# Kernel tuning notes

Measured on AMD Instinct MI355X. Metric: run time of the kernel, lower is better.

## Reference

```python
import jax, jax.numpy as jnp
import numpy as np

BS = 1024
D = 64            # hidden_dim
S = 16            # neighbor_samples
HOPS = 2          # context_hops
AGG = 1.0         # agg_param
N_ENT = 200000
N_EDGE = 2000000
N_REL = 16


def setup_inputs() -> dict:
    key = jax.random.key(0)
    ks = jax.random.split(key, 10)
    return {
        "relations":    jax.random.randint(ks[0], (BS,), 0, N_REL),
        "entity_pairs": jax.random.randint(ks[1], (BS, 2), 0, N_ENT),
        "train_edges":  jax.random.randint(ks[2], (BS,), 0, N_EDGE),
        "entity2edges": jax.random.randint(ks[3], (N_ENT, S), 0, N_EDGE),
        "edge2entities": jax.random.randint(ks[4], (N_EDGE, 2), 0, N_ENT),
        "edge2relation": jax.random.randint(ks[5], (N_EDGE,), 0, N_REL),
        "relation_emb": jax.random.normal(ks[6], (N_REL, D), jnp.float32) * (1.0 / D ** 0.5),
        "entity_emb":   jax.random.normal(ks[7], (N_ENT, D), jnp.float32) * (1.0 / D ** 0.5),
        "scorer_w":     jax.random.normal(ks[8], (D, 1), jnp.float32) * 0.1,
        "scorer_b":     jnp.zeros((1,), jnp.float32),
    }


def reference(relations, entity_pairs, train_edges, entity2edges, edge2entities,
              edge2relation, relation_emb, entity_emb, scorer_w, scorer_b):
    bs = relations.shape[0]
    dtype = relation_emb.dtype

    # ---- _get_entity_neighbors_and_masks (train mode) ----
    edges_list = [relations]          # hop-0 "edges" are the relation ids
    nodes_list = []
    mask_list = []
    te = train_edges[:, None]         # the edge to predict is masked out
    for i in range(HOPS):
        if i == 0:
            neighbor_entities = entity_pairs                      # [bs, 2]
        else:
            # entities at the two endpoints of every previous-hop edge
            neighbor_entities = edge2entities[edges_list[-1]].reshape(bs, -1, 2)
        nodes_list.append(neighbor_entities)
        neighbor_edges = entity2edges[neighbor_entities.reshape(bs, -1)].reshape(bs, -1)
        edges_list.append(neighbor_edges)
        mask_list.append((neighbor_edges != te).astype(dtype))    # (edge - train_edge) != 0

    # ---- embedding lookups ----
    entity_vectors = [entity_emb[n] for n in nodes_list]
    edge_vectors = [relation_emb[edges_list[0]]]                  # [bs, D]
    for edges in edges_list[1:]:
        edge_vectors.append(relation_emb[edge2relation[edges]])

    # ---- iterative MeanAggregator hops (self_included=True) ----
    for i in range(HOPS):
        next_edge_vectors = []
        for hop in range(HOPS - i):
            self_vec = edge_vectors[hop].reshape(bs, -1, D)              # [bs, m, D]
            nev = entity_vectors[hop].reshape(bs, -1, 2, D)              # [bs, m, 2, D]
            nbv = edge_vectors[hop + 1].reshape(bs, -1, 2, S, D)         # [bs, m, 2, S, D]
            m = mask_list[hop].reshape(bs, -1, 2, S, 1)                  # [bs, m, 2, S, 1]
            nei_nums = jnp.sum(m, axis=-2)                               # [bs, m, 2, 1]
            nei_nums = jnp.where(nei_nums == 0, jnp.ones_like(nei_nums), nei_nums)
            edge_agg = jnp.sum(nbv * m, axis=-2) / nei_nums              # masked mean over S
            neighbor_vectors = nev + AGG * edge_agg                      # [bs, m, 2, D]
            self_vec = self_vec + AGG * jnp.mean(neighbor_vectors, axis=-2)
            next_edge_vectors.append(self_vec)
        edge_vectors = next_edge_vectors

    out = edge_vectors[0].reshape(bs, D)
    scores = out @ scorer_w + scorer_b                                   # mlp scorer
    return scores[:, 0]
```

## Files before the change

kernel.cpp:

```cpp
#include <hip/hip_runtime.h>


#define DIM 64
#define NS 16
#define NREL 16

__global__ __launch_bounds__(512, 8) void transmatch_main(
    const int* __restrict__ relations,
    const int* __restrict__ entity_pairs,
    const int* __restrict__ train_edges,
    const int* __restrict__ entity2edges,
    const int* __restrict__ edge2entities,
    const int* __restrict__ edge2relation,
    const float* __restrict__ relation_emb,
    const float* __restrict__ entity_emb,
    const float* __restrict__ scorer_w,
    const float* __restrict__ scorer_b,
    float* __restrict__ out)
{
    __shared__ float RwL[NREL];
    __shared__ float wL[DIM];
    __shared__ int   node_l[64];
    __shared__ int   m0i[32];
    __shared__ float c0s[2];
    __shared__ float ews[2];
    __shared__ float rw0s[2];
    __shared__ float wavesum[8];

    const int b    = blockIdx.x;
    const int t    = threadIdx.x;
    const int lane = t & 63;
    const int wave = t >> 6;
    const int te   = train_edges[b];

    if (t < DIM) wL[t] = scorer_w[t];

    int rel1 = 0, m0 = 0;
    if (wave == 0 && lane < 32) {
        const int p    = lane >> 4;
        const int e    = entity_pairs[b * 2 + p];
        const int edge = entity2edges[e * NS + (lane & 15)];
        m0   = (edge != te) ? 1 : 0;
        rel1 = edge2relation[edge];
        const int2 nn = reinterpret_cast<const int2*>(edge2entities)[edge];
        reinterpret_cast<int2*>(node_l)[lane] = nn;
        m0i[lane] = m0;
        int c = m0;
        c += __shfl_xor(c, 1); c += __shfl_xor(c, 2);
        c += __shfl_xor(c, 4); c += __shfl_xor(c, 8);
        if ((lane & 15) == 0) c0s[p] = (float)c;
    } else if (wave == 1) {
        const int p  = lane >> 5;
        const int e  = entity_pairs[b * 2 + p];
        const int k  = lane & 31;
        const float2 ev = reinterpret_cast<const float2*>(entity_emb)[e * 32 + k];
        float v = ev.x * scorer_w[2 * k] + ev.y * scorer_w[2 * k + 1];
        v += __shfl_xor(v, 1); v += __shfl_xor(v, 2); v += __shfl_xor(v, 4);
        v += __shfl_xor(v, 8); v += __shfl_xor(v, 16);
        if (k == 0) ews[p] = v;
    } else if (wave == 2) {
        const int r = lane >> 2, seg = lane & 3;
        const float4* R4 = reinterpret_cast<const float4*>(relation_emb);
        const float4* W4 = reinterpret_cast<const float4*>(scorer_w);
        float v = 0.0f;
        #pragma unroll
        for (int k = 0; k < 4; ++k) {
            const float4 rr = R4[r * 16 + seg * 4 + k];
            const float4 ww = W4[seg * 4 + k];
            v = fmaf(rr.x, ww.x, v); v = fmaf(rr.y, ww.y, v);
            v = fmaf(rr.z, ww.z, v); v = fmaf(rr.w, ww.w, v);
        }
        v += __shfl_xor(v, 1); v += __shfl_xor(v, 2);
        if (seg == 0) RwL[r] = v;
    }
    __syncthreads();

    if (wave == 0 && lane < 32) {
        float rv = m0 ? RwL[rel1] : 0.0f;
        rv += __shfl_xor(rv, 1); rv += __shfl_xor(rv, 2);
        rv += __shfl_xor(rv, 4); rv += __shfl_xor(rv, 8);
        if ((lane & 15) == 0) rw0s[lane >> 4] = rv;
    }

    {
        const int n    = t >> 3;
        const int h    = t & 7;
        const int node = node_l[n];

        const int2 ed = reinterpret_cast<const int2*>(entity2edges)[node * 8 + h];
        const int ra = edge2relation[ed.x];
        const int rb = edge2relation[ed.y];

        const float4* E4  = reinterpret_cast<const float4*>(entity_emb);
        const float4* wL4 = reinterpret_cast<const float4*>(wL);
        const float4 ev0 = E4[node * 16 + h * 2];
        const float4 ev1 = E4[node * 16 + h * 2 + 1];
        const float4 w0  = wL4[h * 2];
        const float4 w1  = wL4[h * 2 + 1];
        float dotp = 0.0f;
        dotp = fmaf(ev0.x, w0.x, dotp); dotp = fmaf(ev0.y, w0.y, dotp);
        dotp = fmaf(ev0.z, w0.z, dotp); dotp = fmaf(ev0.w, w0.w, dotp);
        dotp = fmaf(ev1.x, w1.x, dotp); dotp = fmaf(ev1.y, w1.y, dotp);
        dotp = fmaf(ev1.z, w1.z, dotp); dotp = fmaf(ev1.w, w1.w, dotp);

        int cnt = 0; float rws = 0.0f;
        if (ed.x != te) { cnt++; rws += RwL[ra]; }
        if (ed.y != te) { cnt++; rws += RwL[rb]; }

        dotp += __shfl_xor(dotp, 1); dotp += __shfl_xor(dotp, 2); dotp += __shfl_xor(dotp, 4);
        rws  += __shfl_xor(rws, 1);  rws  += __shfl_xor(rws, 2);  rws  += __shfl_xor(rws, 4);
        cnt  += __shfl_xor(cnt, 1);  cnt  += __shfl_xor(cnt, 2);  cnt  += __shfl_xor(cnt, 4);

        float v = 0.0f;
        if (h == 0 && m0i[n >> 1])
            v = dotp + rws / (float)max(cnt, 1);

        v += __shfl_xor(v, 8); v += __shfl_xor(v, 16); v += __shfl_xor(v, 32);
        if (lane == 0) wavesum[wave] = v;
    }
    __syncthreads();

    if (t == 0) {
        const float i0 = 1.0f / fmaxf(c0s[0], 1.0f);
        const float i1 = 1.0f / fmaxf(c0s[1], 1.0f);
        const float S0 = wavesum[0] + wavesum[1] + wavesum[2] + wavesum[3];
        const float S1 = wavesum[4] + wavesum[5] + wavesum[6] + wavesum[7];
        const int   r0 = relations[b];
        out[b] = scorer_b[0] + RwL[r0]
               + ews[0] + i0 * rw0s[0] + 0.25f * i0 * S0
               + ews[1] + i1 * rw0s[1] + 0.25f * i1 * S1;
    }
}

extern "C" void kernel_launch(void* const* d_in, const int* in_sizes, int n_in,
                              void* d_out, int out_size, void* d_ws, size_t ws_size,
                              hipStream_t stream) {
    const int*   relations     = (const int*)d_in[0];
    const int*   entity_pairs  = (const int*)d_in[1];
    const int*   train_edges   = (const int*)d_in[2];
    const int*   entity2edges  = (const int*)d_in[3];
    const int*   edge2entities = (const int*)d_in[4];
    const int*   edge2relation = (const int*)d_in[5];
    const float* relation_emb  = (const float*)d_in[6];
    const float* entity_emb    = (const float*)d_in[7];
    const float* scorer_w      = (const float*)d_in[8];
    const float* scorer_b      = (const float*)d_in[9];
    float* out = (float*)d_out;

    const int bs = in_sizes[0];

    transmatch_main<<<bs, 512, 0, stream>>>(
        relations, entity_pairs, train_edges, entity2edges, edge2entities,
        edge2relation, relation_emb, entity_emb, scorer_w, scorer_b, out);
}
```

Before: 24.17 us.

## Pack edge2relation into 4-bit nibbles and use nontemporal gather loads

Adds a pre-pass kernel that compresses the 2M-entry edge2relation table into 4-bit packed words in workspace, so the main kernel's random relation lookups touch a much smaller table. The main kernel's gathers from edge2entities, entity2edges and entity_emb switch to nontemporal loads to reduce cache pollution. In exchange, every call now streams the full 8 MB edge2relation array through an extra kernel, which likely outweighs the savings on a kernel that only does about 1024 blocks of random gathers. The packing also assumes relation ids fit in 4 bits.

```diff
diff --git a/kernel.cpp b/kernel.cpp
--- a/kernel.cpp
+++ b/kernel.cpp
@@ -5,17 +5,48 @@
 #define NS 16
 #define NREL 16
 
-__global__ __launch_bounds__(512, 8) void transmatch_main(
+typedef float f32x4 __attribute__((ext_vector_type(4)));
+typedef int   i32x2 __attribute__((ext_vector_type(2)));
+
+__global__ __launch_bounds__(256) void pack_nib_kernel(
+    const int* __restrict__ e2r, unsigned int* __restrict__ nib, int n) {
+    const int tid = blockIdx.x * blockDim.x + threadIdx.x;
+    const int i = tid * 8;
+    if (i + 7 < n) {
+        const int4 a = *reinterpret_cast<const int4*>(e2r + i);
+        const int4 b = *reinterpret_cast<const int4*>(e2r + i + 4);
+        unsigned int w =  (unsigned int)(a.x & 15)
+                       | ((unsigned int)(a.y & 15) << 4)
+                       | ((unsigned int)(a.z & 15) << 8)
+                       | ((unsigned int)(a.w & 15) << 12)
+                       | ((unsigned int)(b.x & 15) << 16)
+                       | ((unsigned int)(b.y & 15) << 20)
+                       | ((unsigned int)(b.z & 15) << 24)
+                       | ((unsigned int)(b.w & 15) << 28);
+        nib[tid] = w;
+    } else if (i < n) {
+        unsigned int w = 0;
+        for (int k = 0; k < 8 && i + k < n; ++k)
+            w |= ((unsigned int)(e2r[i + k] & 15)) << (4 * k);
+        nib[tid] = w;
+    }
+}
+
+__device__ __forceinline__ int rel4(const unsigned int* __restrict__ nib, int e) {
+    return (int)((nib[e >> 3] >> ((e & 7) << 2)) & 15u);
+}
+
+__global__ __launch_bounds__(512) void transmatch_main(
     const int* __restrict__ relations,
     const int* __restrict__ entity_pairs,
     const int* __restrict__ train_edges,
     const int* __restrict__ entity2edges,
     const int* __restrict__ edge2entities,
-    const int* __restrict__ edge2relation,
     const float* __restrict__ relation_emb,
     const float* __restrict__ entity_emb,
     const float* __restrict__ scorer_w,
     const float* __restrict__ scorer_b,
+    const unsigned int* __restrict__ nib,
     float* __restrict__ out)
 {
     __shared__ float RwL[NREL];
@@ -41,9 +72,11 @@
         const int e    = entity_pairs[b * 2 + p];
         const int edge = entity2edges[e * NS + (lane & 15)];
         m0   = (edge != te) ? 1 : 0;
-        rel1 = edge2relation[edge];
-        const int2 nn = reinterpret_cast<const int2*>(edge2entities)[edge];
-        reinterpret_cast<int2*>(node_l)[lane] = nn;
+        rel1 = rel4(nib, edge);
+        const i32x2 nn = __builtin_nontemporal_load(
+            reinterpret_cast<const i32x2*>(edge2entities) + edge);
+        node_l[2 * lane]     = nn.x;
+        node_l[2 * lane + 1] = nn.y;
         m0i[lane] = m0;
         int c = m0;
         c += __shfl_xor(c, 1); c += __shfl_xor(c, 2);
@@ -87,16 +120,17 @@
         const int h    = t & 7;
         const int node = node_l[n];
 
-        const int2 ed = reinterpret_cast<const int2*>(entity2edges)[node * 8 + h];
-        const int ra = edge2relation[ed.x];
-        const int rb = edge2relation[ed.y];
+        const i32x2 ed = __builtin_nontemporal_load(
+            reinterpret_cast<const i32x2*>(entity2edges) + (node * 8 + h));
+        const int ra = rel4(nib, ed.x);
+        const int rb = rel4(nib, ed.y);
 
-        const float4* E4  = reinterpret_cast<const float4*>(entity_emb);
+        const f32x4* E4 = reinterpret_cast<const f32x4*>(entity_emb);
         const float4* wL4 = reinterpret_cast<const float4*>(wL);
-        const float4 ev0 = E4[node * 16 + h * 2];
-        const float4 ev1 = E4[node * 16 + h * 2 + 1];
-        const float4 w0  = wL4[h * 2];
-        const float4 w1  = wL4[h * 2 + 1];
+        const f32x4 ev0 = __builtin_nontemporal_load(E4 + (node * 16 + h * 2));
+        const f32x4 ev1 = __builtin_nontemporal_load(E4 + (node * 16 + h * 2 + 1));
+        const float4 w0 = wL4[h * 2];
+        const float4 w1 = wL4[h * 2 + 1];
         float dotp = 0.0f;
         dotp = fmaf(ev0.x, w0.x, dotp); dotp = fmaf(ev0.y, w0.y, dotp);
         dotp = fmaf(ev0.z, w0.z, dotp); dotp = fmaf(ev0.w, w0.w, dotp);
@@ -147,9 +181,16 @@
     const float* scorer_b      = (const float*)d_in[9];
     float* out = (float*)d_out;
 
-    const int bs = in_sizes[0];
+    const int bs     = in_sizes[0];
+    const int n_edge = in_sizes[5];
+    const int n_words = (n_edge + 7) / 8;
+
+    unsigned int* nib = (unsigned int*)d_ws;
+    const int pack_threads = n_words;
+    pack_nib_kernel<<<(pack_threads + 255) / 256, 256, 0, stream>>>(
+        edge2relation, nib, n_edge);
 
     transmatch_main<<<bs, 512, 0, stream>>>(
         relations, entity_pairs, train_edges, entity2edges, edge2entities,
-        edge2relation, relation_emb, entity_emb, scorer_w, scorer_b, out);
+        relation_emb, entity_emb, scorer_w, scorer_b, nib, out);
 }
```

After: 22.70 us. 1.07x faster.

## Precompute per-entity relation-score sums to remove per-edge relation gathers

Applied to the files above, without the earlier changes.

Adds a precompute kernel that, for every entity, sums the scorer-projected relation scores of its 16 edges into a workspace table. The main kernel then subtracts the train-edge contribution using a count of matches instead of gathering edge2relation for each neighbor edge. This removes dependent random gathers in the main kernel. In exchange, a full pass over all 200k entities (3.2M random edge2relation reads) runs on every call, which is far more work than the 1024-sample batch needs.

```diff
diff --git a/kernel.cpp b/kernel.cpp
--- a/kernel.cpp
+++ b/kernel.cpp
@@ -4,6 +4,51 @@
 #define DIM 64
 #define NS 16
 #define NREL 16
+
+__global__ __launch_bounds__(256) void rs_precompute(
+    const int* __restrict__ entity2edges,
+    const int* __restrict__ e2r,
+    const float* __restrict__ relation_emb,
+    const float* __restrict__ scorer_w,
+    float* __restrict__ RS,
+    int n_ent)
+{
+    __shared__ float RwL[NREL];
+    const int t = threadIdx.x;
+
+    if (t < 64) {
+        const int r = t >> 2, seg = t & 3;
+        const float4* R4 = reinterpret_cast<const float4*>(relation_emb);
+        const float4* W4 = reinterpret_cast<const float4*>(scorer_w);
+        float v = 0.0f;
+        #pragma unroll
+        for (int k = 0; k < 4; ++k) {
+            const float4 rr = R4[r * 16 + seg * 4 + k];
+            const float4 ww = W4[seg * 4 + k];
+            v = fmaf(rr.x, ww.x, v); v = fmaf(rr.y, ww.y, v);
+            v = fmaf(rr.z, ww.z, v); v = fmaf(rr.w, ww.w, v);
+        }
+        v += __shfl_xor(v, 1); v += __shfl_xor(v, 2);
+        if (seg == 0) RwL[r] = v;
+    }
+    __syncthreads();
+
+    const int n = blockIdx.x * 256 + t;
+    if (n < n_ent) {
+        const int4* row = reinterpret_cast<const int4*>(entity2edges + (size_t)n * NS);
+        const int4 a = row[0], b = row[1], c = row[2], d = row[3];
+        float rs = 0.0f;
+        rs += RwL[e2r[a.x] & 15]; rs += RwL[e2r[a.y] & 15];
+        rs += RwL[e2r[a.z] & 15]; rs += RwL[e2r[a.w] & 15];
+        rs += RwL[e2r[b.x] & 15]; rs += RwL[e2r[b.y] & 15];
+        rs += RwL[e2r[b.z] & 15]; rs += RwL[e2r[b.w] & 15];
+        rs += RwL[e2r[c.x] & 15]; rs += RwL[e2r[c.y] & 15];
+        rs += RwL[e2r[c.z] & 15]; rs += RwL[e2r[c.w] & 15];
+        rs += RwL[e2r[d.x] & 15]; rs += RwL[e2r[d.y] & 15];
+        rs += RwL[e2r[d.z] & 15]; rs += RwL[e2r[d.w] & 15];
+        RS[n] = rs;
+    }
+}
 
 __global__ __launch_bounds__(512, 8) void transmatch_main(
     const int* __restrict__ relations,
@@ -11,11 +56,12 @@
     const int* __restrict__ train_edges,
     const int* __restrict__ entity2edges,
     const int* __restrict__ edge2entities,
-    const int* __restrict__ edge2relation,
+    const int* __restrict__ e2r,
     const float* __restrict__ relation_emb,
     const float* __restrict__ entity_emb,
     const float* __restrict__ scorer_w,
     const float* __restrict__ scorer_b,
+    const float* __restrict__ RS,
     float* __restrict__ out)
 {
     __shared__ float RwL[NREL];
@@ -24,7 +70,8 @@
     __shared__ int   m0i[32];
     __shared__ float c0s[2];
     __shared__ float ews[2];
-    __shared__ float rw0s[2];
+    __shared__ float rsp[2];
+    __shared__ int   srte;
     __shared__ float wavesum[8];
 
     const int b    = blockIdx.x;
@@ -35,13 +82,11 @@
 
     if (t < DIM) wL[t] = scorer_w[t];
 
-    int rel1 = 0, m0 = 0;
     if (wave == 0 && lane < 32) {
         const int p    = lane >> 4;
         const int e    = entity_pairs[b * 2 + p];
         const int edge = entity2edges[e * NS + (lane & 15)];
-        m0   = (edge != te) ? 1 : 0;
-        rel1 = edge2relation[edge];
+        const int m0   = (edge != te) ? 1 : 0;
         const int2 nn = reinterpret_cast<const int2*>(edge2entities)[edge];
         reinterpret_cast<int2*>(node_l)[lane] = nn;
         m0i[lane] = m0;
@@ -57,7 +102,7 @@
         float v = ev.x * scorer_w[2 * k] + ev.y * scorer_w[2 * k + 1];
         v += __shfl_xor(v, 1); v += __shfl_xor(v, 2); v += __shfl_xor(v, 4);
         v += __shfl_xor(v, 8); v += __shfl_xor(v, 16);
-        if (k == 0) ews[p] = v;
+        if (k == 0) { ews[p] = v; rsp[p] = RS[e]; }
     } else if (wave == 2) {
         const int r = lane >> 2, seg = lane & 3;
         const float4* R4 = reinterpret_cast<const float4*>(relation_emb);
@@ -72,15 +117,10 @@
         }
         v += __shfl_xor(v, 1); v += __shfl_xor(v, 2);
         if (seg == 0) RwL[r] = v;
+    } else if (wave == 3) {
+        if (lane == 0) srte = e2r[te] & 15;
     }
     __syncthreads();
-
-    if (wave == 0 && lane < 32) {
-        float rv = m0 ? RwL[rel1] : 0.0f;
-        rv += __shfl_xor(rv, 1); rv += __shfl_xor(rv, 2);
-        rv += __shfl_xor(rv, 4); rv += __shfl_xor(rv, 8);
-        if ((lane & 15) == 0) rw0s[lane >> 4] = rv;
-    }
 
     {
         const int n    = t >> 3;
@@ -88,8 +128,7 @@
         const int node = node_l[n];
 
         const int2 ed = reinterpret_cast<const int2*>(entity2edges)[node * 8 + h];
-        const int ra = edge2relation[ed.x];
-        const int rb = edge2relation[ed.y];
+        int matches = ((ed.x == te) ? 1 : 0) + ((ed.y == te) ? 1 : 0);
 
         const float4* E4  = reinterpret_cast<const float4*>(entity_emb);
         const float4* wL4 = reinterpret_cast<const float4*>(wL);
@@ -103,17 +142,16 @@
         dotp = fmaf(ev1.x, w1.x, dotp); dotp = fmaf(ev1.y, w1.y, dotp);
         dotp = fmaf(ev1.z, w1.z, dotp); dotp = fmaf(ev1.w, w1.w, dotp);
 
-        int cnt = 0; float rws = 0.0f;
-        if (ed.x != te) { cnt++; rws += RwL[ra]; }
-        if (ed.y != te) { cnt++; rws += RwL[rb]; }
-
-        dotp += __shfl_xor(dotp, 1); dotp += __shfl_xor(dotp, 2); dotp += __shfl_xor(dotp, 4);
-        rws  += __shfl_xor(rws, 1);  rws  += __shfl_xor(rws, 2);  rws  += __shfl_xor(rws, 4);
-        cnt  += __shfl_xor(cnt, 1);  cnt  += __shfl_xor(cnt, 2);  cnt  += __shfl_xor(cnt, 4);
+        dotp    += __shfl_xor(dotp, 1); dotp    += __shfl_xor(dotp, 2); dotp    += __shfl_xor(dotp, 4);
+        matches += __shfl_xor(matches, 1); matches += __shfl_xor(matches, 2); matches += __shfl_xor(matches, 4);
 
         float v = 0.0f;
-        if (h == 0 && m0i[n >> 1])
+        if (h == 0 && m0i[n >> 1]) {
+            const float rwte = RwL[srte];
+            const float rws  = RS[node] - (float)matches * rwte;
+            const int   cnt  = NS - matches;
             v = dotp + rws / (float)max(cnt, 1);
+        }
 
         v += __shfl_xor(v, 8); v += __shfl_xor(v, 16); v += __shfl_xor(v, 32);
         if (lane == 0) wavesum[wave] = v;
@@ -121,14 +159,17 @@
     __syncthreads();
 
     if (t == 0) {
+        const float rwte = RwL[srte];
         const float i0 = 1.0f / fmaxf(c0s[0], 1.0f);
         const float i1 = 1.0f / fmaxf(c0s[1], 1.0f);
+        const float rw00 = rsp[0] - (16.0f - c0s[0]) * rwte;
+        const float rw01 = rsp[1] - (16.0f - c0s[1]) * rwte;
         const float S0 = wavesum[0] + wavesum[1] + wavesum[2] + wavesum[3];
         const float S1 = wavesum[4] + wavesum[5] + wavesum[6] + wavesum[7];
         const int   r0 = relations[b];
         out[b] = scorer_b[0] + RwL[r0]
-               + ews[0] + i0 * rw0s[0] + 0.25f * i0 * S0
-               + ews[1] + i1 * rw0s[1] + 0.25f * i1 * S1;
+               + ews[0] + i0 * rw00 + 0.25f * i0 * S0
+               + ews[1] + i1 * rw01 + 0.25f * i1 * S1;
     }
 }
 
@@ -147,9 +188,15 @@
     const float* scorer_b      = (const float*)d_in[9];
     float* out = (float*)d_out;
 
-    const int bs = in_sizes[0];
+    const int bs    = in_sizes[0];
+    const int n_ent = in_sizes[3] / NS;
+
+    float* RS = (float*)d_ws;
+
+    rs_precompute<<<(n_ent + 255) / 256, 256, 0, stream>>>(
+        entity2edges, edge2relation, relation_emb, scorer_w, RS, n_ent);
 
     transmatch_main<<<bs, 512, 0, stream>>>(
         relations, entity_pairs, train_edges, entity2edges, edge2entities,
-        edge2relation, relation_emb, entity_emb, scorer_w, scorer_b, out);
+        edge2relation, relation_emb, entity_emb, scorer_w, scorer_b, RS, out);
 }
```

After: 48.16 us. 1.99x slower.
